# Kernel optimization log

Hardware: AMD Instinct MI355X
Metric: run time of the kernel (lower is better)

## Reference

```python
import jax, jax.numpy as jnp
import numpy as np

B, Q, K, D, H = 2, 2048, 2048, 1024, 16
HD = D // H  # 64
EPS = 1e-6  # flax LayerNorm default epsilon


def setup_inputs() -> dict:
    key = jax.random.key(0)
    ks = jax.random.split(key, 12)
    s = 1.0 / np.sqrt(D)  # lecun_normal-like scale
    inputs_q = jax.random.normal(ks[0], (B, Q, D), jnp.float32)
    bias = jax.random.normal(ks[1], (B, 1, Q, K), jnp.float32)
    mask = jax.random.randint(ks[2], (B, 1, Q, K), 0, 2).astype(jnp.bool_)
    wq = jax.random.normal(ks[3], (D, H, HD), jnp.float32) * s
    wk = jax.random.normal(ks[4], (D, H, HD), jnp.float32) * s
    wv = jax.random.normal(ks[5], (D, H, HD), jnp.float32) * s
    bq = jnp.zeros((H, HD), jnp.float32)
    bk = jnp.zeros((H, HD), jnp.float32)
    bv = jnp.zeros((H, HD), jnp.float32)
    q_scale = jnp.ones((HD,), jnp.float32)
    k_scale = jnp.ones((HD,), jnp.float32)
    wo = jax.random.normal(ks[6], (H, HD, D), jnp.float32) * s
    bo = jnp.zeros((D,), jnp.float32)
    return dict(inputs_q=inputs_q, bias=bias, mask=mask, wq=wq, bq=bq,
                wk=wk, bk=bk, wv=wv, bv=bv, q_scale=q_scale, k_scale=k_scale,
                wo=wo, bo=bo)


def _layernorm_nobias(x, scale):
    # normalize over last axis (head_dim), no bias, like flax LayerNorm(use_bias=False)
    mean = jnp.mean(x, axis=-1, keepdims=True)
    var = jnp.mean(jnp.square(x - mean), axis=-1, keepdims=True)
    return (x - mean) * jax.lax.rsqrt(var + EPS) * scale


def reference(inputs_q, bias, mask, wq, bq, wk, bk, wv, bv, q_scale, k_scale, wo, bo):
    # QKV projections (self-attention: k and v inputs default to inputs_q)
    q = jnp.einsum('bqd,dhe->bqhe', inputs_q, wq) + bq  # [B,Q,H,HD]
    k = jnp.einsum('bkd,dhe->bkhe', inputs_q, wk) + bk  # [B,K,H,HD]
    v = jnp.einsum('bkd,dhe->bkhe', inputs_q, wv) + bv  # [B,K,H,HD]
    # optional QK layernorm (normalize_qk=True)
    q = _layernorm_nobias(q, q_scale)
    k = _layernorm_nobias(k, k_scale)
    # attention weights
    q = q / jnp.sqrt(jnp.asarray(q.shape[-1], q.dtype))
    attn = jnp.einsum('bqhe,bkhe->bhqk', q, k)  # [B,H,Q,K]
    attn = attn + bias
    big_neg = jnp.finfo(q.dtype).min
    attn = jnp.where(mask, attn, big_neg)
    attn = jax.nn.softmax(attn.astype(jnp.float32), axis=-1).astype(q.dtype)
    # weighted values + output projection
    x = jnp.einsum('bhqk,bkhe->bqhe', attn, v)  # [B,Q,H,HD]
    out = jnp.einsum('bqhe,heo->bqo', x, wo) + bo  # [B,Q,D]
    return out
```

## Files before the change

### kernel.cpp

```cpp
#include <hip/hip_runtime.h>
#include <cstdint>
#include <cstddef>

typedef __bf16 bf16_t;
typedef __bf16 bf16x8 __attribute__((ext_vector_type(8)));
typedef __bf16 bf16x4 __attribute__((ext_vector_type(4)));
typedef _Float16 f16_t;
typedef _Float16 f16x4 __attribute__((ext_vector_type(4)));
typedef float f32x4 __attribute__((ext_vector_type(4)));

constexpr int BB = 2, SS = 2048, DD = 1024, HH = 16, HDIM = 64;
constexpr int BS = BB * SS;
constexpr float LOG2E = 1.4426950408889634f;

__global__ void convert_x(const float* __restrict__ src, bf16_t* __restrict__ dst, int n4) {
  int i = blockIdx.x * blockDim.x + threadIdx.x;
  if (i >= n4) return;
  float4 v = ((const float4*)src)[i];
  union { bf16_t h[4]; uint2 u; } o;
  o.h[0] = (bf16_t)v.x; o.h[1] = (bf16_t)v.y; o.h[2] = (bf16_t)v.z; o.h[3] = (bf16_t)v.w;
  ((uint2*)dst)[i] = o.u;
}

__global__ void transpose_convert(const float* __restrict__ wq, const float* __restrict__ wk,
                                  const float* __restrict__ wv, const float* __restrict__ wo,
                                  bf16_t* __restrict__ wqkv_t, bf16_t* __restrict__ wo_t) {
  int which = blockIdx.z;
  const float* src = (which == 0) ? wq : (which == 1) ? wk : (which == 2) ? wv : wo;
  bf16_t* dst = (which < 3) ? wqkv_t : wo_t;
  int noff = (which < 3) ? which * 1024 : 0;
  __shared__ float tile[64][65];
  int tr = blockIdx.y, tc = blockIdx.x;
  int t = threadIdx.x;
#pragma unroll
  for (int p = 0; p < 4; ++p) {
    int e = (p * 256 + t) * 4;
    int r = e >> 6, c = e & 63;
    float4 v = *(const float4*)&src[(size_t)(tr * 64 + r) * 1024 + tc * 64 + c];
    tile[r][c] = v.x; tile[r][c + 1] = v.y; tile[r][c + 2] = v.z; tile[r][c + 3] = v.w;
  }
  __syncthreads();
#pragma unroll
  for (int p = 0; p < 4; ++p) {
    int e = (p * 256 + t) * 4;
    int r = e >> 6, c = e & 63;
    union { bf16_t h[4]; uint2 u; } o;
#pragma unroll
    for (int j = 0; j < 4; ++j) o.h[j] = (bf16_t)tile[c + j][r];
    *(uint2*)&dst[(size_t)(noff + tc * 64 + r) * 1024 + tr * 64 + c] = o.u;
  }
}

__global__ void prep_biasmask(const float* __restrict__ bias, const int* __restrict__ mask,
                              bf16_t* __restrict__ bmq) {
  int i = blockIdx.x * blockDim.x + threadIdx.x;
  float4 b0 = ((const float4*)bias)[i * 2];
  float4 b1 = ((const float4*)bias)[i * 2 + 1];
  int4 m0 = ((const int4*)mask)[i * 2];
  int4 m1 = ((const int4*)mask)[i * 2 + 1];
  union { bf16_t h[8]; uint4 u; } o;
  o.h[0] = (bf16_t)(m0.x ? b0.x * LOG2E - 8.0f : -2.0e38f);
  o.h[1] = (bf16_t)(m0.y ? b0.y * LOG2E - 8.0f : -2.0e38f);
  o.h[2] = (bf16_t)(m0.z ? b0.z * LOG2E - 8.0f : -2.0e38f);
  o.h[3] = (bf16_t)(m0.w ? b0.w * LOG2E - 8.0f : -2.0e38f);
  o.h[4] = (bf16_t)(m1.x ? b1.x * LOG2E - 8.0f : -2.0e38f);
  o.h[5] = (bf16_t)(m1.y ? b1.y * LOG2E - 8.0f : -2.0e38f);
  o.h[6] = (bf16_t)(m1.z ? b1.z * LOG2E - 8.0f : -2.0e38f);
  o.h[7] = (bf16_t)(m1.w ? b1.w * LOG2E - 8.0f : -2.0e38f);
  ((uint4*)bmq)[i] = o.u;
}

__global__ void vt_relayout(const bf16_t* __restrict__ Cqkv, const float* __restrict__ bv,
                            f16_t* __restrict__ vt) {
  __shared__ float tile[64][65];
  int st = blockIdx.x, h = blockIdx.y, b = blockIdx.z;
  int t = threadIdx.x;
#pragma unroll
  for (int p = 0; p < 2; ++p) {
    int e = (p * 256 + t) * 8;
    int r = e >> 6, c = e & 63;
    bf16x8 v8 = *(const bf16x8*)&Cqkv[(size_t)(b * SS + st * 64 + r) * 3072 + 2048 + h * 64 + c];
#pragma unroll
    for (int j = 0; j < 8; ++j) tile[r][c + j] = (float)v8[j] + bv[h * 64 + c + j];
  }
  __syncthreads();
#pragma unroll
  for (int p = 0; p < 2; ++p) {
    int e = (p * 256 + t) * 8;
    int r = e >> 6, c = e & 63;
    union { f16_t h[8]; uint4 u; } o;
#pragma unroll
    for (int j = 0; j < 8; ++j) o.h[j] = (f16_t)tile[c + j][r];
    *(uint4*)&vt[(size_t)((b * HH + h) * HDIM + r) * SS + st * 64 + c] = o.u;
  }
}

template <bool OUT_F32>
__global__ __launch_bounds__(256) void gemm_bt(const bf16_t* __restrict__ A,
                                               const bf16_t* __restrict__ Bt,
                                               bf16_t* __restrict__ Cb, float* __restrict__ Cf,
                                               const float* __restrict__ bias, int M, int N,
                                               int Kd) {
  __shared__ __align__(16) bf16_t As[128][72];
  __shared__ __align__(16) bf16_t Bs[128][72];
  int tid = threadIdx.x;
  int lane = tid & 63, w = tid >> 6;
  int lo = lane & 15, quad = lane >> 4;
  int wm = w >> 1, wn = w & 1;
  int m0 = blockIdx.y * 128, n0 = blockIdx.x * 128;
  f32x4 acc[4][4] = {};
  for (int kk = 0; kk < Kd; kk += 64) {
#pragma unroll
    for (int p = 0; p < 4; ++p) {
      int idx = (p * 256 + tid) * 8;
      int r = idx >> 6, c = idx & 63;
      *(bf16x8*)&As[r][c] = *(const bf16x8*)&A[(size_t)(m0 + r) * Kd + kk + c];
      *(bf16x8*)&Bs[r][c] = *(const bf16x8*)&Bt[(size_t)(n0 + r) * Kd + kk + c];
    }
    __syncthreads();
#pragma unroll
    for (int kc = 0; kc < 2; ++kc) {
      bf16x8 am[4], bn[4];
#pragma unroll
      for (int i = 0; i < 4; ++i)
        am[i] = *(const bf16x8*)&As[wm * 64 + i * 16 + lo][kc * 32 + quad * 8];
#pragma unroll
      for (int i = 0; i < 4; ++i)
        bn[i] = *(const bf16x8*)&Bs[wn * 64 + i * 16 + lo][kc * 32 + quad * 8];
#pragma unroll
      for (int mi = 0; mi < 4; ++mi)
#pragma unroll
        for (int ni = 0; ni < 4; ++ni)
          acc[mi][ni] = __builtin_amdgcn_mfma_f32_16x16x32_bf16(am[mi], bn[ni], acc[mi][ni], 0, 0, 0);
    }
    __syncthreads();
  }
#pragma unroll
  for (int mi = 0; mi < 4; ++mi) {
#pragma unroll
    for (int ni = 0; ni < 4; ++ni) {
#pragma unroll
      for (int r = 0; r < 4; ++r) {
        int row = m0 + wm * 64 + mi * 16 + quad * 4 + r;
        int col = n0 + wn * 64 + ni * 16 + lo;
        float v = acc[mi][ni][r];
        if (OUT_F32)
          Cf[(size_t)row * N + col] = v + bias[col];
        else
          Cb[(size_t)row * N + col] = (bf16_t)v;
      }
    }
  }
}

__global__ void ln_relayout(const bf16_t* __restrict__ Cqkv, const float* __restrict__ bq,
                            const float* __restrict__ bk, const float* __restrict__ q_scale,
                            const float* __restrict__ k_scale, bf16_t* __restrict__ qb,
                            bf16_t* __restrict__ kb) {
  int mode = blockIdx.y;
  int vec = blockIdx.x * 4 + (threadIdx.x >> 6);
  int lane = threadIdx.x & 63;
  int bs = vec >> 4, h = vec & 15;
  int b = bs >> 11, s = bs & 2047;
  const float* badd = (mode == 0) ? bq : bk;
  float x = (float)Cqkv[(size_t)bs * 3072 + mode * 1024 + h * 64 + lane] + badd[h * 64 + lane];
  float sum = x;
#pragma unroll
  for (int off = 32; off >= 1; off >>= 1) sum += __shfl_xor(sum, off, 64);
  float mean = sum * (1.0f / 64.0f);
  float d = x - mean;
  float vs = d * d;
#pragma unroll
  for (int off = 32; off >= 1; off >>= 1) vs += __shfl_xor(vs, off, 64);
  float var = vs * (1.0f / 64.0f);
  const float* sc = (mode == 0) ? q_scale : k_scale;
  float y = d * rsqrtf(var + 1e-6f) * sc[lane];
  if (mode == 0) y *= 0.125f * LOG2E;
  bf16_t* dst = (mode == 0) ? qb : kb;
  dst[(size_t)((b * 16 + h) * 2048 + s) * 64 + lane] = (bf16_t)y;
}

__global__ __launch_bounds__(256) void attn_kernel(const bf16_t* __restrict__ qb,
                                                   const bf16_t* __restrict__ kb,
                                                   const f16_t* __restrict__ vt,
                                                   const bf16_t* __restrict__ bmq,
                                                   bf16_t* __restrict__ xout) {
  __shared__ __align__(16) bf16_t Ks[64][72];
  __shared__ __align__(16) f16_t Vs[64][72];
  __shared__ __align__(16) bf16_t Bm[128][72];
  int tid = threadIdx.x;
  int lane = tid & 63, w = tid >> 6;
  int lo = lane & 15, quad = lane >> 4;
  int qt = blockIdx.x, h = blockIdx.y, b = blockIdx.z;
  size_t headoff = (size_t)(b * HH + h) * SS * HDIM;
  int q0b = qt * 128;
  int q0 = q0b + w * 32;
  const bf16_t* kbase = kb + headoff;
  const f16_t* vbase = vt + headoff;
  const bf16_t* bmbase = bmq + (size_t)b * SS * SS;

  bf16x8 bqf[2][2];
#pragma unroll
  for (int qg = 0; qg < 2; ++qg)
#pragma unroll
    for (int ec = 0; ec < 2; ++ec)
      bqf[qg][ec] =
          *(const bf16x8*)&qb[headoff + (size_t)(q0 + qg * 16 + lo) * HDIM + ec * 32 + quad * 8];

  f16x4 ones;
#pragma unroll
  for (int j = 0; j < 4; ++j) ones[j] = (f16_t)1.0f;

  f32x4 ot[2][4] = {};
  f32x4 lacc[2] = {};

  for (int kt = 0; kt < SS / 64; ++kt) {
    int k0 = kt * 64;
#pragma unroll
    for (int p = 0; p < 2; ++p) {
      int idx = (p * 256 + tid) * 8;
      int r = idx >> 6, c = idx & 63;
      *(uint4*)&Ks[r][c] = *(const uint4*)&kbase[(size_t)(k0 + r) * HDIM + c];
      *(uint4*)&Vs[r][c] = *(const uint4*)&vbase[(size_t)r * SS + k0 + c];
    }
#pragma unroll
    for (int p = 0; p < 4; ++p) {
      int idx = (p * 256 + tid) * 8;
      int r = idx >> 6, c = idx & 63;
      *(uint4*)&Bm[r][c] = *(const uint4*)&bmbase[(size_t)(q0b + r) * SS + k0 + c];
    }
    __syncthreads();

    bf16x8 ka[4][2];
#pragma unroll
    for (int mb = 0; mb < 4; ++mb)
#pragma unroll
      for (int ec = 0; ec < 2; ++ec)
        ka[mb][ec] = *(const bf16x8*)&Ks[mb * 16 + lo][ec * 32 + quad * 8];

    f16x4 pf[2][4];
#pragma unroll
    for (int qg = 0; qg < 2; ++qg) {
#pragma unroll
      for (int mb = 0; mb < 4; ++mb) {
        bf16x4 bm4 = *(const bf16x4*)&Bm[w * 32 + qg * 16 + lo][mb * 16 + quad * 4];
        f32x4 s;
#pragma unroll
        for (int r = 0; r < 4; ++r) s[r] = (float)bm4[r];
        s = __builtin_amdgcn_mfma_f32_16x16x32_bf16(ka[mb][0], bqf[qg][0], s, 0, 0, 0);
        s = __builtin_amdgcn_mfma_f32_16x16x32_bf16(ka[mb][1], bqf[qg][1], s, 0, 0, 0);
#pragma unroll
        for (int r = 0; r < 4; ++r) pf[qg][mb][r] = (f16_t)__builtin_amdgcn_exp2f(s[r]);
      }
    }

#pragma unroll
    for (int mb = 0; mb < 4; ++mb) {
#pragma unroll
      for (int eb = 0; eb < 4; ++eb) {
        f16x4 va = *(const f16x4*)&Vs[eb * 16 + lo][mb * 16 + quad * 4];
#pragma unroll
        for (int qg = 0; qg < 2; ++qg)
          ot[qg][eb] = __builtin_amdgcn_mfma_f32_16x16x16f16(va, pf[qg][mb], ot[qg][eb], 0, 0, 0);
      }
#pragma unroll
      for (int qg = 0; qg < 2; ++qg)
        lacc[qg] = __builtin_amdgcn_mfma_f32_16x16x16f16(ones, pf[qg][mb], lacc[qg], 0, 0, 0);
    }
    __syncthreads();
  }

#pragma unroll
  for (int qg = 0; qg < 2; ++qg) {
    float rl = 1.0f / lacc[qg][0];
    int q = q0 + qg * 16 + lo;
#pragma unroll
    for (int eb = 0; eb < 4; ++eb) {
      union { bf16_t h4[4]; uint2 u; } o;
#pragma unroll
      for (int r = 0; r < 4; ++r) o.h4[r] = (bf16_t)(ot[qg][eb][r] * rl);
      *(uint2*)&xout[(size_t)(b * SS + q) * DD + h * 64 + eb * 16 + quad * 4] = o.u;
    }
  }
}

extern "C" void kernel_launch(void* const* d_in, const int* in_sizes, int n_in, void* d_out,
                              int out_size, void* d_ws, size_t ws_size, hipStream_t stream) {
  const float* inputs_q = (const float*)d_in[0];
  const float* bias = (const float*)d_in[1];
  const int* mask = (const int*)d_in[2];
  const float* wq = (const float*)d_in[3];
  const float* bq = (const float*)d_in[4];
  const float* wk = (const float*)d_in[5];
  const float* bk = (const float*)d_in[6];
  const float* wv = (const float*)d_in[7];
  const float* bv = (const float*)d_in[8];
  const float* q_scale = (const float*)d_in[9];
  const float* k_scale = (const float*)d_in[10];
  const float* wo = (const float*)d_in[11];
  const float* bo = (const float*)d_in[12];
  float* out = (float*)d_out;

  char* ws = (char*)d_ws;
  bf16_t* xb     = (bf16_t*)(ws);
  bf16_t* wqkv_t = (bf16_t*)(ws + ((size_t)8 << 20));
  bf16_t* wo_t   = (bf16_t*)(ws + ((size_t)14 << 20));
  bf16_t* cqkv   = (bf16_t*)(ws + ((size_t)16 << 20));
  bf16_t* bmq    = (bf16_t*)(ws + ((size_t)16 << 20));
  bf16_t* qb2    = (bf16_t*)(ws + ((size_t)40 << 20));
  bf16_t* kb2    = (bf16_t*)(ws + ((size_t)48 << 20));
  f16_t*  vtb    = (f16_t*)(ws + ((size_t)56 << 20));
  bf16_t* xattn  = (bf16_t*)(ws + ((size_t)64 << 20));

  convert_x<<<(BS * DD / 4 + 255) / 256, 256, 0, stream>>>(inputs_q, xb, BS * DD / 4);
  transpose_convert<<<dim3(16, 16, 4), 256, 0, stream>>>(wq, wk, wv, wo, wqkv_t, wo_t);
  gemm_bt<false><<<dim3(24, 32), 256, 0, stream>>>(xb, wqkv_t, cqkv, nullptr, nullptr, BS, 3072, DD);
  ln_relayout<<<dim3(BS * HH / 4, 2), 256, 0, stream>>>(cqkv, bq, bk, q_scale, k_scale, qb2, kb2);
  vt_relayout<<<dim3(32, 16, 2), 256, 0, stream>>>(cqkv, bv, vtb);
  prep_biasmask<<<BB * SS * SS / 8 / 256, 256, 0, stream>>>(bias, mask, bmq);
  attn_kernel<<<dim3(SS / 128, HH, BB), 256, 0, stream>>>(qb2, kb2, vtb, bmq, xattn);
  gemm_bt<true><<<dim3(8, 32), 256, 0, stream>>>(xattn, wo_t, nullptr, out, bo, BS, 1024, DD);
}
```

Before: 307.3 us.

## Use direct global-to-LDS loads in GEMM and widen attention blocks to 512 threads

Measured after the change: 310.6 us. Within noise of the previous version (+1.1%).

```diff
diff --git a/kernel.cpp b/kernel.cpp
--- a/kernel.cpp
+++ b/kernel.cpp
@@ -12,6 +12,11 @@
 constexpr int BB = 2, SS = 2048, DD = 1024, HH = 16, HDIM = 64;
 constexpr int BS = BB * SS;
 constexpr float LOG2E = 1.4426950408889634f;
+
+__device__ __forceinline__ void glds16(const void* g, void* l) {
+  __builtin_amdgcn_global_load_lds((const __attribute__((address_space(1))) void*)g,
+                                   (__attribute__((address_space(3))) void*)l, 16, 0, 0);
+}
 
 __global__ void convert_x(const float* __restrict__ src, bf16_t* __restrict__ dst, int n4) {
   int i = blockIdx.x * blockDim.x + threadIdx.x;
@@ -101,38 +106,35 @@
                                                bf16_t* __restrict__ Cb, float* __restrict__ Cf,
                                                const float* __restrict__ bias, int M, int N,
                                                int Kd) {
-  __shared__ __align__(16) bf16_t As[128][72];
-  __shared__ __align__(16) bf16_t Bs[128][72];
+  __shared__ __align__(16) bf16_t As[128][32];
+  __shared__ __align__(16) bf16_t Bs[128][32];
   int tid = threadIdx.x;
   int lane = tid & 63, w = tid >> 6;
   int lo = lane & 15, quad = lane >> 4;
   int wm = w >> 1, wn = w & 1;
   int m0 = blockIdx.y * 128, n0 = blockIdx.x * 128;
+  int srow = lane >> 2;
+  int scol = (lane & 3) * 8;
   f32x4 acc[4][4] = {};
-  for (int kk = 0; kk < Kd; kk += 64) {
-#pragma unroll
-    for (int p = 0; p < 4; ++p) {
-      int idx = (p * 256 + tid) * 8;
-      int r = idx >> 6, c = idx & 63;
-      *(bf16x8*)&As[r][c] = *(const bf16x8*)&A[(size_t)(m0 + r) * Kd + kk + c];
-      *(bf16x8*)&Bs[r][c] = *(const bf16x8*)&Bt[(size_t)(n0 + r) * Kd + kk + c];
-    }
+  for (int kk = 0; kk < Kd; kk += 32) {
+#pragma unroll
+    for (int t = 0; t < 2; ++t) {
+      int rb = (w * 2 + t) * 16;
+      glds16(&A[(size_t)(m0 + rb + srow) * Kd + kk + scol], &As[rb][0]);
+      glds16(&Bt[(size_t)(n0 + rb + srow) * Kd + kk + scol], &Bs[rb][0]);
+    }
+    asm volatile("s_waitcnt vmcnt(0)" ::: "memory");
     __syncthreads();
-#pragma unroll
-    for (int kc = 0; kc < 2; ++kc) {
-      bf16x8 am[4], bn[4];
-#pragma unroll
-      for (int i = 0; i < 4; ++i)
-        am[i] = *(const bf16x8*)&As[wm * 64 + i * 16 + lo][kc * 32 + quad * 8];
-#pragma unroll
-      for (int i = 0; i < 4; ++i)
-        bn[i] = *(const bf16x8*)&Bs[wn * 64 + i * 16 + lo][kc * 32 + quad * 8];
-#pragma unroll
-      for (int mi = 0; mi < 4; ++mi)
-#pragma unroll
-        for (int ni = 0; ni < 4; ++ni)
-          acc[mi][ni] = __builtin_amdgcn_mfma_f32_16x16x32_bf16(am[mi], bn[ni], acc[mi][ni], 0, 0, 0);
-    }
+    bf16x8 am[4], bn[4];
+#pragma unroll
+    for (int i = 0; i < 4; ++i) am[i] = *(const bf16x8*)&As[wm * 64 + i * 16 + lo][quad * 8];
+#pragma unroll
+    for (int i = 0; i < 4; ++i) bn[i] = *(const bf16x8*)&Bs[wn * 64 + i * 16 + lo][quad * 8];
+#pragma unroll
+    for (int mi = 0; mi < 4; ++mi)
+#pragma unroll
+      for (int ni = 0; ni < 4; ++ni)
+        acc[mi][ni] = __builtin_amdgcn_mfma_f32_16x16x32_bf16(am[mi], bn[ni], acc[mi][ni], 0, 0, 0);
     __syncthreads();
   }
 #pragma unroll
@@ -180,7 +182,7 @@
   dst[(size_t)((b * 16 + h) * 2048 + s) * 64 + lane] = (bf16_t)y;
 }
 
-__global__ __launch_bounds__(256) void attn_kernel(const bf16_t* __restrict__ qb,
+__global__ __launch_bounds__(512) void attn_kernel(const bf16_t* __restrict__ qb,
                                                    const bf16_t* __restrict__ kb,
                                                    const f16_t* __restrict__ vt,
                                                    const bf16_t* __restrict__ bmq,
@@ -194,38 +196,33 @@
   int qt = blockIdx.x, h = blockIdx.y, b = blockIdx.z;
   size_t headoff = (size_t)(b * HH + h) * SS * HDIM;
   int q0b = qt * 128;
-  int q0 = q0b + w * 32;
+  int qw = q0b + w * 16;
   const bf16_t* kbase = kb + headoff;
   const f16_t* vbase = vt + headoff;
   const bf16_t* bmbase = bmq + (size_t)b * SS * SS;
 
-  bf16x8 bqf[2][2];
-#pragma unroll
-  for (int qg = 0; qg < 2; ++qg)
-#pragma unroll
-    for (int ec = 0; ec < 2; ++ec)
-      bqf[qg][ec] =
-          *(const bf16x8*)&qb[headoff + (size_t)(q0 + qg * 16 + lo) * HDIM + ec * 32 + quad * 8];
+  bf16x8 bqf[2];
+#pragma unroll
+  for (int ec = 0; ec < 2; ++ec)
+    bqf[ec] = *(const bf16x8*)&qb[headoff + (size_t)(qw + lo) * HDIM + ec * 32 + quad * 8];
 
   f16x4 ones;
 #pragma unroll
   for (int j = 0; j < 4; ++j) ones[j] = (f16_t)1.0f;
 
-  f32x4 ot[2][4] = {};
-  f32x4 lacc[2] = {};
+  f32x4 ot[4] = {};
+  f32x4 lacc = {};
+
+  int sr = tid >> 3;
+  int sc8 = (tid & 7) * 8;
 
   for (int kt = 0; kt < SS / 64; ++kt) {
     int k0 = kt * 64;
+    *(uint4*)&Ks[sr][sc8] = *(const uint4*)&kbase[(size_t)(k0 + sr) * HDIM + sc8];
+    *(uint4*)&Vs[sr][sc8] = *(const uint4*)&vbase[(size_t)sr * SS + k0 + sc8];
 #pragma unroll
     for (int p = 0; p < 2; ++p) {
-      int idx = (p * 256 + tid) * 8;
-      int r = idx >> 6, c = idx & 63;
-      *(uint4*)&Ks[r][c] = *(const uint4*)&kbase[(size_t)(k0 + r) * HDIM + c];
-      *(uint4*)&Vs[r][c] = *(const uint4*)&vbase[(size_t)r * SS + k0 + c];
-    }
-#pragma unroll
-    for (int p = 0; p < 4; ++p) {
-      int idx = (p * 256 + tid) * 8;
+      int idx = (p * 512 + tid) * 8;
       int r = idx >> 6, c = idx & 63;
       *(uint4*)&Bm[r][c] = *(const uint4*)&bmbase[(size_t)(q0b + r) * SS + k0 + c];
     }
@@ -238,20 +235,17 @@
       for (int ec = 0; ec < 2; ++ec)
         ka[mb][ec] = *(const bf16x8*)&Ks[mb * 16 + lo][ec * 32 + quad * 8];
 
-    f16x4 pf[2][4];
-#pragma unroll
-    for (int qg = 0; qg < 2; ++qg) {
-#pragma unroll
-      for (int mb = 0; mb < 4; ++mb) {
-        bf16x4 bm4 = *(const bf16x4*)&Bm[w * 32 + qg * 16 + lo][mb * 16 + quad * 4];
-        f32x4 s;
-#pragma unroll
-        for (int r = 0; r < 4; ++r) s[r] = (float)bm4[r];
-        s = __builtin_amdgcn_mfma_f32_16x16x32_bf16(ka[mb][0], bqf[qg][0], s, 0, 0, 0);
-        s = __builtin_amdgcn_mfma_f32_16x16x32_bf16(ka[mb][1], bqf[qg][1], s, 0, 0, 0);
-#pragma unroll
-        for (int r = 0; r < 4; ++r) pf[qg][mb][r] = (f16_t)__builtin_amdgcn_exp2f(s[r]);
-      }
+    f16x4 pf[4];
+#pragma unroll
+    for (int mb = 0; mb < 4; ++mb) {
+      bf16x4 bm4 = *(const bf16x4*)&Bm[w * 16 + lo][mb * 16 + quad * 4];
+      f32x4 s;
+#pragma unroll
+      for (int r = 0; r < 4; ++r) s[r] = (float)bm4[r];
+      s = __builtin_amdgcn_mfma_f32_16x16x32_bf16(ka[mb][0], bqf[0], s, 0, 0, 0);
+      s = __builtin_amdgcn_mfma_f32_16x16x32_bf16(ka[mb][1], bqf[1], s, 0, 0, 0);
+#pragma unroll
+      for (int r = 0; r < 4; ++r) pf[mb][r] = (f16_t)__builtin_amdgcn_exp2f(s[r]);
     }
 
 #pragma unroll
@@ -259,28 +253,21 @@
 #pragma unroll
       for (int eb = 0; eb < 4; ++eb) {
         f16x4 va = *(const f16x4*)&Vs[eb * 16 + lo][mb * 16 + quad * 4];
-#pragma unroll
-        for (int qg = 0; qg < 2; ++qg)
-          ot[qg][eb] = __builtin_amdgcn_mfma_f32_16x16x16f16(va, pf[qg][mb], ot[qg][eb], 0, 0, 0);
+        ot[eb] = __builtin_amdgcn_mfma_f32_16x16x16f16(va, pf[mb], ot[eb], 0, 0, 0);
       }
-#pragma unroll
-      for (int qg = 0; qg < 2; ++qg)
-        lacc[qg] = __builtin_amdgcn_mfma_f32_16x16x16f16(ones, pf[qg][mb], lacc[qg], 0, 0, 0);
+      lacc = __builtin_amdgcn_mfma_f32_16x16x16f16(ones, pf[mb], lacc, 0, 0, 0);
     }
     __syncthreads();
   }
 
-#pragma unroll
-  for (int qg = 0; qg < 2; ++qg) {
-    float rl = 1.0f / lacc[qg][0];
-    int q = q0 + qg * 16 + lo;
-#pragma unroll
-    for (int eb = 0; eb < 4; ++eb) {
-      union { bf16_t h4[4]; uint2 u; } o;
-#pragma unroll
-      for (int r = 0; r < 4; ++r) o.h4[r] = (bf16_t)(ot[qg][eb][r] * rl);
-      *(uint2*)&xout[(size_t)(b * SS + q) * DD + h * 64 + eb * 16 + quad * 4] = o.u;
-    }
+  float rl = 1.0f / lacc[0];
+  int q = qw + lo;
+#pragma unroll
+  for (int eb = 0; eb < 4; ++eb) {
+    union { bf16_t h4[4]; uint2 u; } o;
+#pragma unroll
+    for (int r = 0; r < 4; ++r) o.h4[r] = (bf16_t)(ot[eb][r] * rl);
+    *(uint2*)&xout[(size_t)(b * SS + q) * DD + h * 64 + eb * 16 + quad * 4] = o.u;
   }
 }
 
@@ -318,6 +305,6 @@
   ln_relayout<<<dim3(BS * HH / 4, 2), 256, 0, stream>>>(cqkv, bq, bk, q_scale, k_scale, qb2, kb2);
   vt_relayout<<<dim3(32, 16, 2), 256, 0, stream>>>(cqkv, bv, vtb);
   prep_biasmask<<<BB * SS * SS / 8 / 256, 256, 0, stream>>>(bias, mask, bmq);
-  attn_kernel<<<dim3(SS / 128, HH, BB), 256, 0, stream>>>(qb2, kb2, vtb, bmq, xattn);
+  attn_kernel<<<dim3(SS / 128, HH, BB), 512, 0, stream>>>(qb2, kb2, vtb, bmq, xattn);
   gemm_bt<true><<<dim3(8, 32), 256, 0, stream>>>(xattn, wo_t, nullptr, out, bo, BS, 1024, DD);
 }
```

## Fuse prep and post-QKV kernels, use global_load_lds in GEMM, repack workspace

Applied to the files above, without the earlier changes.

Measured after the change: 300.7 us. 1.02x faster.

```diff
diff --git a/kernel.cpp b/kernel.cpp
--- a/kernel.cpp
+++ b/kernel.cpp
@@ -13,85 +13,64 @@
 constexpr int BS = BB * SS;
 constexpr float LOG2E = 1.4426950408889634f;
 
-__global__ void convert_x(const float* __restrict__ src, bf16_t* __restrict__ dst, int n4) {
-  int i = blockIdx.x * blockDim.x + threadIdx.x;
-  if (i >= n4) return;
-  float4 v = ((const float4*)src)[i];
-  union { bf16_t h[4]; uint2 u; } o;
-  o.h[0] = (bf16_t)v.x; o.h[1] = (bf16_t)v.y; o.h[2] = (bf16_t)v.z; o.h[3] = (bf16_t)v.w;
-  ((uint2*)dst)[i] = o.u;
-}
-
-__global__ void transpose_convert(const float* __restrict__ wq, const float* __restrict__ wk,
-                                  const float* __restrict__ wv, const float* __restrict__ wo,
-                                  bf16_t* __restrict__ wqkv_t, bf16_t* __restrict__ wo_t) {
-  int which = blockIdx.z;
-  const float* src = (which == 0) ? wq : (which == 1) ? wk : (which == 2) ? wv : wo;
-  bf16_t* dst = (which < 3) ? wqkv_t : wo_t;
-  int noff = (which < 3) ? which * 1024 : 0;
+__device__ __forceinline__ void glds16(const void* g, void* l) {
+  __builtin_amdgcn_global_load_lds((const __attribute__((address_space(1))) void*)g,
+                                   (__attribute__((address_space(3))) void*)l, 16, 0, 0);
+}
+
+__global__ __launch_bounds__(256) void prep_fused(
+    const float* __restrict__ x, const float* __restrict__ wq, const float* __restrict__ wk,
+    const float* __restrict__ wv, const float* __restrict__ wo, const float* __restrict__ bias,
+    const int* __restrict__ mask, bf16_t* __restrict__ xb, bf16_t* __restrict__ wqkv_t,
+    bf16_t* __restrict__ wo_t, bf16_t* __restrict__ bmq) {
   __shared__ float tile[64][65];
-  int tr = blockIdx.y, tc = blockIdx.x;
+  int bid = blockIdx.x;
   int t = threadIdx.x;
-#pragma unroll
-  for (int p = 0; p < 4; ++p) {
-    int e = (p * 256 + t) * 4;
-    int r = e >> 6, c = e & 63;
-    float4 v = *(const float4*)&src[(size_t)(tr * 64 + r) * 1024 + tc * 64 + c];
-    tile[r][c] = v.x; tile[r][c + 1] = v.y; tile[r][c + 2] = v.z; tile[r][c + 3] = v.w;
-  }
-  __syncthreads();
-#pragma unroll
-  for (int p = 0; p < 4; ++p) {
-    int e = (p * 256 + t) * 4;
-    int r = e >> 6, c = e & 63;
+  if (bid < 4096) {
+    int i = bid * 256 + t;
+    float4 v = ((const float4*)x)[i];
     union { bf16_t h[4]; uint2 u; } o;
-#pragma unroll
-    for (int j = 0; j < 4; ++j) o.h[j] = (bf16_t)tile[c + j][r];
-    *(uint2*)&dst[(size_t)(noff + tc * 64 + r) * 1024 + tr * 64 + c] = o.u;
-  }
-}
-
-__global__ void prep_biasmask(const float* __restrict__ bias, const int* __restrict__ mask,
-                              bf16_t* __restrict__ bmq) {
-  int i = blockIdx.x * blockDim.x + threadIdx.x;
-  float4 b0 = ((const float4*)bias)[i * 2];
-  float4 b1 = ((const float4*)bias)[i * 2 + 1];
-  int4 m0 = ((const int4*)mask)[i * 2];
-  int4 m1 = ((const int4*)mask)[i * 2 + 1];
-  union { bf16_t h[8]; uint4 u; } o;
-  o.h[0] = (bf16_t)(m0.x ? b0.x * LOG2E - 8.0f : -2.0e38f);
-  o.h[1] = (bf16_t)(m0.y ? b0.y * LOG2E - 8.0f : -2.0e38f);
-  o.h[2] = (bf16_t)(m0.z ? b0.z * LOG2E - 8.0f : -2.0e38f);
-  o.h[3] = (bf16_t)(m0.w ? b0.w * LOG2E - 8.0f : -2.0e38f);
-  o.h[4] = (bf16_t)(m1.x ? b1.x * LOG2E - 8.0f : -2.0e38f);
-  o.h[5] = (bf16_t)(m1.y ? b1.y * LOG2E - 8.0f : -2.0e38f);
-  o.h[6] = (bf16_t)(m1.z ? b1.z * LOG2E - 8.0f : -2.0e38f);
-  o.h[7] = (bf16_t)(m1.w ? b1.w * LOG2E - 8.0f : -2.0e38f);
-  ((uint4*)bmq)[i] = o.u;
-}
-
-__global__ void vt_relayout(const bf16_t* __restrict__ Cqkv, const float* __restrict__ bv,
-                            f16_t* __restrict__ vt) {
-  __shared__ float tile[64][65];
-  int st = blockIdx.x, h = blockIdx.y, b = blockIdx.z;
-  int t = threadIdx.x;
-#pragma unroll
-  for (int p = 0; p < 2; ++p) {
-    int e = (p * 256 + t) * 8;
-    int r = e >> 6, c = e & 63;
-    bf16x8 v8 = *(const bf16x8*)&Cqkv[(size_t)(b * SS + st * 64 + r) * 3072 + 2048 + h * 64 + c];
-#pragma unroll
-    for (int j = 0; j < 8; ++j) tile[r][c + j] = (float)v8[j] + bv[h * 64 + c + j];
-  }
-  __syncthreads();
-#pragma unroll
-  for (int p = 0; p < 2; ++p) {
-    int e = (p * 256 + t) * 8;
-    int r = e >> 6, c = e & 63;
-    union { f16_t h[8]; uint4 u; } o;
-#pragma unroll
-    for (int j = 0; j < 8; ++j) o.h[j] = (f16_t)tile[c + j][r];
-    *(uint4*)&vt[(size_t)((b * HH + h) * HDIM + r) * SS + st * 64 + c] = o.u;
+    o.h[0] = (bf16_t)v.x; o.h[1] = (bf16_t)v.y; o.h[2] = (bf16_t)v.z; o.h[3] = (bf16_t)v.w;
+    ((uint2*)xb)[i] = o.u;
+  } else if (bid < 5120) {
+    int id = bid - 4096;
+    int which = id >> 8, tr = (id >> 4) & 15, tc = id & 15;
+    const float* src = (which == 0) ? wq : (which == 1) ? wk : (which == 2) ? wv : wo;
+    bf16_t* dst = (which < 3) ? wqkv_t : wo_t;
+    int noff = (which < 3) ? which * 1024 : 0;
+#pragma unroll
+    for (int p = 0; p < 4; ++p) {
+      int e = (p * 256 + t) * 4;
+      int r = e >> 6, c = e & 63;
+      float4 v = *(const float4*)&src[(size_t)(tr * 64 + r) * 1024 + tc * 64 + c];
+      tile[r][c] = v.x; tile[r][c + 1] = v.y; tile[r][c + 2] = v.z; tile[r][c + 3] = v.w;
+    }
+    __syncthreads();
+#pragma unroll
+    for (int p = 0; p < 4; ++p) {
+      int e = (p * 256 + t) * 4;
+      int r = e >> 6, c = e & 63;
+      union { bf16_t h[4]; uint2 u; } o;
+#pragma unroll
+      for (int j = 0; j < 4; ++j) o.h[j] = (bf16_t)tile[c + j][r];
+      *(uint2*)&dst[(size_t)(noff + tc * 64 + r) * 1024 + tr * 64 + c] = o.u;
+    }
+  } else {
+    int i = (bid - 5120) * 256 + t;
+    float4 b0 = ((const float4*)bias)[i * 2];
+    float4 b1 = ((const float4*)bias)[i * 2 + 1];
+    int4 m0 = ((const int4*)mask)[i * 2];
+    int4 m1 = ((const int4*)mask)[i * 2 + 1];
+    union { bf16_t h[8]; uint4 u; } o;
+    o.h[0] = (bf16_t)(m0.x ? b0.x * LOG2E - 8.0f : -2.0e38f);
+    o.h[1] = (bf16_t)(m0.y ? b0.y * LOG2E - 8.0f : -2.0e38f);
+    o.h[2] = (bf16_t)(m0.z ? b0.z * LOG2E - 8.0f : -2.0e38f);
+    o.h[3] = (bf16_t)(m0.w ? b0.w * LOG2E - 8.0f : -2.0e38f);
+    o.h[4] = (bf16_t)(m1.x ? b1.x * LOG2E - 8.0f : -2.0e38f);
+    o.h[5] = (bf16_t)(m1.y ? b1.y * LOG2E - 8.0f : -2.0e38f);
+    o.h[6] = (bf16_t)(m1.z ? b1.z * LOG2E - 8.0f : -2.0e38f);
+    o.h[7] = (bf16_t)(m1.w ? b1.w * LOG2E - 8.0f : -2.0e38f);
+    ((uint4*)bmq)[i] = o.u;
   }
 }
 
@@ -101,38 +80,35 @@
                                                bf16_t* __restrict__ Cb, float* __restrict__ Cf,
                                                const float* __restrict__ bias, int M, int N,
                                                int Kd) {
-  __shared__ __align__(16) bf16_t As[128][72];
-  __shared__ __align__(16) bf16_t Bs[128][72];
+  __shared__ __align__(16) bf16_t As[128][32];
+  __shared__ __align__(16) bf16_t Bs[128][32];
   int tid = threadIdx.x;
   int lane = tid & 63, w = tid >> 6;
   int lo = lane & 15, quad = lane >> 4;
   int wm = w >> 1, wn = w & 1;
   int m0 = blockIdx.y * 128, n0 = blockIdx.x * 128;
+  int srow = lane >> 2;
+  int scol = (lane & 3) * 8;
   f32x4 acc[4][4] = {};
-  for (int kk = 0; kk < Kd; kk += 64) {
-#pragma unroll
-    for (int p = 0; p < 4; ++p) {
-      int idx = (p * 256 + tid) * 8;
-      int r = idx >> 6, c = idx & 63;
-      *(bf16x8*)&As[r][c] = *(const bf16x8*)&A[(size_t)(m0 + r) * Kd + kk + c];
-      *(bf16x8*)&Bs[r][c] = *(const bf16x8*)&Bt[(size_t)(n0 + r) * Kd + kk + c];
-    }
-    __syncthreads();
-#pragma unroll
-    for (int kc = 0; kc < 2; ++kc) {
-      bf16x8 am[4], bn[4];
-#pragma unroll
-      for (int i = 0; i < 4; ++i)
-        am[i] = *(const bf16x8*)&As[wm * 64 + i * 16 + lo][kc * 32 + quad * 8];
-#pragma unroll
-      for (int i = 0; i < 4; ++i)
-        bn[i] = *(const bf16x8*)&Bs[wn * 64 + i * 16 + lo][kc * 32 + quad * 8];
-#pragma unroll
-      for (int mi = 0; mi < 4; ++mi)
-#pragma unroll
-        for (int ni = 0; ni < 4; ++ni)
-          acc[mi][ni] = __builtin_amdgcn_mfma_f32_16x16x32_bf16(am[mi], bn[ni], acc[mi][ni], 0, 0, 0);
-    }
+  for (int kk = 0; kk < Kd; kk += 32) {
+#pragma unroll
+    for (int t = 0; t < 2; ++t) {
+      int rb = (w * 2 + t) * 16;
+      glds16(&A[(size_t)(m0 + rb + srow) * Kd + kk + scol], &As[rb][0]);
+      glds16(&Bt[(size_t)(n0 + rb + srow) * Kd + kk + scol], &Bs[rb][0]);
+    }
+    asm volatile("s_waitcnt vmcnt(0)" ::: "memory");
+    __syncthreads();
+    bf16x8 am[4], bn[4];
+#pragma unroll
+    for (int i = 0; i < 4; ++i) am[i] = *(const bf16x8*)&As[wm * 64 + i * 16 + lo][quad * 8];
+#pragma unroll
+    for (int i = 0; i < 4; ++i) bn[i] = *(const bf16x8*)&Bs[wn * 64 + i * 16 + lo][quad * 8];
+#pragma unroll
+    for (int mi = 0; mi < 4; ++mi)
+#pragma unroll
+      for (int ni = 0; ni < 4; ++ni)
+        acc[mi][ni] = __builtin_amdgcn_mfma_f32_16x16x32_bf16(am[mi], bn[ni], acc[mi][ni], 0, 0, 0);
     __syncthreads();
   }
 #pragma unroll
@@ -153,31 +129,61 @@
   }
 }
 
-__global__ void ln_relayout(const bf16_t* __restrict__ Cqkv, const float* __restrict__ bq,
-                            const float* __restrict__ bk, const float* __restrict__ q_scale,
-                            const float* __restrict__ k_scale, bf16_t* __restrict__ qb,
-                            bf16_t* __restrict__ kb) {
-  int mode = blockIdx.y;
-  int vec = blockIdx.x * 4 + (threadIdx.x >> 6);
-  int lane = threadIdx.x & 63;
-  int bs = vec >> 4, h = vec & 15;
-  int b = bs >> 11, s = bs & 2047;
-  const float* badd = (mode == 0) ? bq : bk;
-  float x = (float)Cqkv[(size_t)bs * 3072 + mode * 1024 + h * 64 + lane] + badd[h * 64 + lane];
-  float sum = x;
-#pragma unroll
-  for (int off = 32; off >= 1; off >>= 1) sum += __shfl_xor(sum, off, 64);
-  float mean = sum * (1.0f / 64.0f);
-  float d = x - mean;
-  float vs = d * d;
-#pragma unroll
-  for (int off = 32; off >= 1; off >>= 1) vs += __shfl_xor(vs, off, 64);
-  float var = vs * (1.0f / 64.0f);
-  const float* sc = (mode == 0) ? q_scale : k_scale;
-  float y = d * rsqrtf(var + 1e-6f) * sc[lane];
-  if (mode == 0) y *= 0.125f * LOG2E;
-  bf16_t* dst = (mode == 0) ? qb : kb;
-  dst[(size_t)((b * 16 + h) * 2048 + s) * 64 + lane] = (bf16_t)y;
+__global__ __launch_bounds__(256) void postqkv(const bf16_t* __restrict__ Cqkv,
+                                               const float* __restrict__ bq,
+                                               const float* __restrict__ bk,
+                                               const float* __restrict__ bv,
+                                               const float* __restrict__ q_scale,
+                                               const float* __restrict__ k_scale,
+                                               bf16_t* __restrict__ qb, bf16_t* __restrict__ kb,
+                                               f16_t* __restrict__ vt) {
+  __shared__ float tile[64][65];
+  int bid = blockIdx.x;
+  int t = threadIdx.x;
+  if (bid < 32768) {
+    int mode = bid >> 14;
+    int vec = (bid & 16383) * 4 + (t >> 6);
+    int lane = t & 63;
+    int bs = vec >> 4, h = vec & 15;
+    int b = bs >> 11, s = bs & 2047;
+    const float* badd = (mode == 0) ? bq : bk;
+    float x = (float)Cqkv[(size_t)bs * 3072 + mode * 1024 + h * 64 + lane] + badd[h * 64 + lane];
+    float sum = x;
+#pragma unroll
+    for (int off = 32; off >= 1; off >>= 1) sum += __shfl_xor(sum, off, 64);
+    float mean = sum * (1.0f / 64.0f);
+    float d = x - mean;
+    float vs = d * d;
+#pragma unroll
+    for (int off = 32; off >= 1; off >>= 1) vs += __shfl_xor(vs, off, 64);
+    float var = vs * (1.0f / 64.0f);
+    const float* sc = (mode == 0) ? q_scale : k_scale;
+    float y = d * rsqrtf(var + 1e-6f) * sc[lane];
+    if (mode == 0) y *= 0.125f * LOG2E;
+    bf16_t* dst = (mode == 0) ? qb : kb;
+    dst[(size_t)((b * 16 + h) * 2048 + s) * 64 + lane] = (bf16_t)y;
+  } else {
+    int id2 = bid - 32768;
+    int st = id2 & 31, h = (id2 >> 5) & 15, b = id2 >> 9;
+#pragma unroll
+    for (int p = 0; p < 2; ++p) {
+      int e = (p * 256 + t) * 8;
+      int r = e >> 6, c = e & 63;
+      bf16x8 v8 = *(const bf16x8*)&Cqkv[(size_t)(b * SS + st * 64 + r) * 3072 + 2048 + h * 64 + c];
+#pragma unroll
+      for (int j = 0; j < 8; ++j) tile[r][c + j] = (float)v8[j] + bv[h * 64 + c + j];
+    }
+    __syncthreads();
+#pragma unroll
+    for (int p = 0; p < 2; ++p) {
+      int e = (p * 256 + t) * 8;
+      int r = e >> 6, c = e & 63;
+      union { f16_t h[8]; uint4 u; } o;
+#pragma unroll
+      for (int j = 0; j < 8; ++j) o.h[j] = (f16_t)tile[c + j][r];
+      *(uint4*)&vt[(size_t)((b * HH + h) * HDIM + r) * SS + st * 64 + c] = o.u;
+    }
+  }
 }
 
 __global__ __launch_bounds__(256) void attn_kernel(const bf16_t* __restrict__ qb,
@@ -302,22 +308,19 @@
   float* out = (float*)d_out;
 
   char* ws = (char*)d_ws;
-  bf16_t* xb     = (bf16_t*)(ws);
-  bf16_t* wqkv_t = (bf16_t*)(ws + ((size_t)8 << 20));
-  bf16_t* wo_t   = (bf16_t*)(ws + ((size_t)14 << 20));
-  bf16_t* cqkv   = (bf16_t*)(ws + ((size_t)16 << 20));
-  bf16_t* bmq    = (bf16_t*)(ws + ((size_t)16 << 20));
-  bf16_t* qb2    = (bf16_t*)(ws + ((size_t)40 << 20));
-  bf16_t* kb2    = (bf16_t*)(ws + ((size_t)48 << 20));
-  f16_t*  vtb    = (f16_t*)(ws + ((size_t)56 << 20));
-  bf16_t* xattn  = (bf16_t*)(ws + ((size_t)64 << 20));
-
-  convert_x<<<(BS * DD / 4 + 255) / 256, 256, 0, stream>>>(inputs_q, xb, BS * DD / 4);
-  transpose_convert<<<dim3(16, 16, 4), 256, 0, stream>>>(wq, wk, wv, wo, wqkv_t, wo_t);
+  bf16_t* wo_t   = (bf16_t*)(ws);
+  bf16_t* bmq    = (bf16_t*)(ws + ((size_t)2 << 20));
+  bf16_t* cqkv   = (bf16_t*)(ws + ((size_t)19 << 20));
+  bf16_t* xattn  = (bf16_t*)(ws + ((size_t)19 << 20));
+  bf16_t* xb     = (bf16_t*)(ws + ((size_t)43 << 20));
+  bf16_t* qb2    = (bf16_t*)(ws + ((size_t)43 << 20));
+  bf16_t* wqkv_t = (bf16_t*)(ws + ((size_t)51 << 20));
+  bf16_t* kb2    = (bf16_t*)(ws + ((size_t)51 << 20));
+  f16_t*  vtb    = (f16_t*)(ws + ((size_t)59 << 20));
+
+  prep_fused<<<9216, 256, 0, stream>>>(inputs_q, wq, wk, wv, wo, bias, mask, xb, wqkv_t, wo_t, bmq);
   gemm_bt<false><<<dim3(24, 32), 256, 0, stream>>>(xb, wqkv_t, cqkv, nullptr, nullptr, BS, 3072, DD);
-  ln_relayout<<<dim3(BS * HH / 4, 2), 256, 0, stream>>>(cqkv, bq, bk, q_scale, k_scale, qb2, kb2);
-  vt_relayout<<<dim3(32, 16, 2), 256, 0, stream>>>(cqkv, bv, vtb);
-  prep_biasmask<<<BB * SS * SS / 8 / 256, 256, 0, stream>>>(bias, mask, bmq);
+  postqkv<<<33792, 256, 0, stream>>>(cqkv, bq, bk, bv, q_scale, k_scale, qb2, kb2, vtb);
   attn_kernel<<<dim3(SS / 128, HH, BB), 256, 0, stream>>>(qb2, kb2, vtb, bmq, xattn);
   gemm_bt<true><<<dim3(8, 32), 256, 0, stream>>>(xattn, wo_t, nullptr, out, bo, BS, 1024, DD);
 }
```
